# Kernel tuning notes

Measured on AMD Instinct MI355X. Metric: run time of the kernel, lower is better.

Reference implementation:

```python
import jax, jax.numpy as jnp
import numpy as np


def setup_inputs() -> dict:
    key = jax.random.key(0)
    k1, k2, k3, k4 = jax.random.split(key, 4)
    B, S, D = 32, 512, 768
    return {
        "image": jax.random.normal(k1, (B, S, D), dtype=jnp.float32),
        "text": jax.random.normal(k2, (B, S, D), dtype=jnp.float32),
        "target": jax.random.normal(k3, (B, S, D), dtype=jnp.float32),
        "padding_mask": jax.random.randint(k4, (B, S), 0, 2, dtype=jnp.int32),
    }


def reference(image, text, target, padding_mask):
    D = image.shape[-1]
    # Drop BOS / CLS position for the text<->target alignment.
    txt = text[:, 1:]                      # [B, S-1, D]
    tgt = target[:, 1:]                    # [B, S-1, D]
    pm = padding_mask[:, 1:]               # [B, S-1]

    # Cosine similarity: normalize then batched matmul.
    txt_n = txt / jnp.linalg.norm(txt, axis=-1, keepdims=True)
    tgt_n = tgt / jnp.linalg.norm(tgt, axis=-1, keepdims=True)
    sim = jnp.einsum('bid,bjd->bij', txt_n, tgt_n)   # [B, S-1, S-1]

    # For each text token, pick the best-matching target patch.
    idx = jnp.argmax(sim, axis=-1)                   # [B, S-1]
    aligned = jnp.take_along_axis(tgt, idx[..., None], axis=1)  # [B, S-1, D]

    # Masked MSE over non-padded tokens (mask==1 means padded in torch code).
    valid = (pm == 0).astype(jnp.float32)            # [B, S-1]
    diff2 = jnp.square(txt.astype(jnp.float32) - aligned.astype(jnp.float32))
    kd_text_loss = jnp.sum(diff2 * valid[..., None]) / (jnp.sum(valid) * D)

    # Plain MSE between image tokens and full target.
    kd_image_loss = jnp.mean(jnp.square(image.astype(jnp.float32) - target.astype(jnp.float32)))

    total_loss = (kd_text_loss + kd_image_loss) / 2
    return total_loss, kd_text_loss, kd_image_loss, idx
```

## Files before the change

kernel.cpp:

```cpp
#include <hip/hip_runtime.h>
#include <math.h>

#define B       32
#define S_FULL  512
#define S       511
#define D       768
#define NROWS   (B * S)

#define TM 128
#define TN 128
#define NCHUNK 4
#define NKT 24
#define RSTR 72
#define EPS_MARGIN 6e-5f

typedef __attribute__((ext_vector_type(8))) short bf16x8;
typedef __attribute__((ext_vector_type(4))) float f32x4;

__device__ inline unsigned short f2bf(float f) {
    union { float f; unsigned u; } c; c.f = f;
    unsigned u = c.u;
    return (unsigned short)((u + 0x7fffu + ((u >> 16) & 1u)) >> 16);
}
__device__ inline float bf2f(unsigned short h) {
    union { unsigned u; float f; } c; c.u = ((unsigned)h) << 16;
    return c.f;
}
__device__ inline void split4(float x0, float x1, float x2, float x3,
                              short4& hi, short4& lo) {
    unsigned short h0 = f2bf(x0), h1 = f2bf(x1), h2 = f2bf(x2), h3 = f2bf(x3);
    hi = make_short4((short)h0, (short)h1, (short)h2, (short)h3);
    lo = make_short4((short)f2bf(x0 - bf2f(h0)), (short)f2bf(x1 - bf2f(h1)),
                     (short)f2bf(x2 - bf2f(h2)), (short)f2bf(x3 - bf2f(h3)));
}

__global__ __launch_bounds__(256) void prep_kernel(
    const float* __restrict__ image, const float* __restrict__ text,
    const float* __restrict__ target,
    float* __restrict__ inv_t, float* __restrict__ inv_g, float* __restrict__ acc)
{
    int row  = blockIdx.x * 4 + (threadIdx.x >> 6);
    int lane = threadIdx.x & 63;
    int b = row >> 9, i = row & 511;
    const float4* pi4 = (const float4*)(image  + (size_t)row * D);
    const float4* pt4 = (const float4*)(text   + (size_t)row * D);
    const float4* pg4 = (const float4*)(target + (size_t)row * D);
    float st = 0.f, sg = 0.f, si = 0.f;
    #pragma unroll
    for (int q = 0; q < 3; ++q) {
        float4 a = pt4[lane + 64 * q];
        float4 g = pg4[lane + 64 * q];
        float4 m = pi4[lane + 64 * q];
        st += a.x*a.x + a.y*a.y + a.z*a.z + a.w*a.w;
        sg += g.x*g.x + g.y*g.y + g.z*g.z + g.w*g.w;
        float dx = m.x-g.x, dy = m.y-g.y, dz = m.z-g.z, dw = m.w-g.w;
        si += dx*dx + dy*dy + dz*dz + dw*dw;
    }
    #pragma unroll
    for (int m = 32; m > 0; m >>= 1) {
        st += __shfl_xor(st, m); sg += __shfl_xor(sg, m); si += __shfl_xor(si, m);
    }
    if (lane == 0) {
        atomicAdd(&acc[blockIdx.x & 63], si);
        if (i >= 1) {
            int r = b * S + i - 1;
            inv_t[r] = (st > 0.f) ? 1.f / sqrtf(st) : 0.f;
            inv_g[r] = (sg > 0.f) ? 1.f / sqrtf(sg) : 0.f;
        }
    }
}

__global__ __launch_bounds__(256, 2) void simargmax_kernel(
    const float* __restrict__ text, const float* __restrict__ target,
    const float* __restrict__ inv_t, const float* __restrict__ inv_g,
    float* __restrict__ pv, float* __restrict__ ps, int* __restrict__ pj)
{
    __shared__ __align__(16) short As[TM * RSTR];
    __shared__ __align__(16) short Bs[TM * RSTR];

    const int i0 = blockIdx.x * TM;
    const int jc = blockIdx.y;
    const int j0 = jc * TN;
    const int b  = blockIdx.z;
    const int t  = threadIdx.x;
    const int lane = t & 63;
    const int wy = t >> 6;
    const int quad = lane >> 4, cid = lane & 15;

    const float* Abase = text   + (size_t)b * S_FULL * D + D;
    const float* Bbase = target + (size_t)b * S_FULL * D + D;

    const int r0 = t >> 3;
    const int kq = (t & 7) * 4;

    float sa[4], sb[4];
    #pragma unroll
    for (int h = 0; h < 4; ++h) {
        int gi = i0 + r0 + h * 32;
        sa[h] = (gi < S) ? inv_t[b * S + gi] : 0.f;
        int gj = j0 + r0 + h * 32;
        sb[h] = (gj < S) ? inv_g[b * S + gj] : 0.f;
    }

    f32x4 acc[2][8];
    #pragma unroll
    for (int mt = 0; mt < 2; ++mt)
        #pragma unroll
        for (int nt = 0; nt < 8; ++nt)
            acc[mt][nt] = (f32x4){0.f, 0.f, 0.f, 0.f};

    for (int kt = 0; kt < NKT; ++kt) {
        const int k0 = kt * 32;
        float4 va[4], vb[4];
        #pragma unroll
        for (int h = 0; h < 4; ++h) {
            int gi = i0 + r0 + h * 32;
            va[h] = (gi < S) ? *(const float4*)(Abase + (size_t)gi * D + k0 + kq)
                             : make_float4(0.f, 0.f, 0.f, 0.f);
            int gj = j0 + r0 + h * 32;
            vb[h] = (gj < S) ? *(const float4*)(Bbase + (size_t)gj * D + k0 + kq)
                             : make_float4(0.f, 0.f, 0.f, 0.f);
        }
        __syncthreads();
        #pragma unroll
        for (int h = 0; h < 4; ++h) {
            int row = r0 + h * 32;
            short4 ahi, alo, bhi, blo;
            split4(va[h].x * sa[h], va[h].y * sa[h], va[h].z * sa[h], va[h].w * sa[h], ahi, alo);
            split4(vb[h].x * sb[h], vb[h].y * sb[h], vb[h].z * sb[h], vb[h].w * sb[h], bhi, blo);
            *(short4*)&As[row * RSTR + kq]      = ahi;
            *(short4*)&As[row * RSTR + 32 + kq] = alo;
            *(short4*)&Bs[row * RSTR + kq]      = bhi;
            *(short4*)&Bs[row * RSTR + 32 + kq] = blo;
        }
        __syncthreads();

        bf16x8 ah[2], al[2];
        #pragma unroll
        for (int mt = 0; mt < 2; ++mt) {
            int ad = (wy * 32 + mt * 16 + cid) * RSTR + quad * 8;
            ah[mt] = *(const bf16x8*)&As[ad];
            al[mt] = *(const bf16x8*)&As[ad + 32];
        }
        #pragma unroll
        for (int nt = 0; nt < 8; ++nt) {
            int bd = (nt * 16 + cid) * RSTR + quad * 8;
            bf16x8 bh = *(const bf16x8*)&Bs[bd];
            bf16x8 bl = *(const bf16x8*)&Bs[bd + 32];
            #pragma unroll
            for (int mt = 0; mt < 2; ++mt) {
                acc[mt][nt] = __builtin_amdgcn_mfma_f32_16x16x32_bf16(ah[mt], bh, acc[mt][nt], 0, 0, 0);
                acc[mt][nt] = __builtin_amdgcn_mfma_f32_16x16x32_bf16(ah[mt], bl, acc[mt][nt], 0, 0, 0);
                acc[mt][nt] = __builtin_amdgcn_mfma_f32_16x16x32_bf16(al[mt], bh, acc[mt][nt], 0, 0, 0);
            }
        }
    }

    #pragma unroll
    for (int mt = 0; mt < 2; ++mt) {
        #pragma unroll
        for (int r = 0; r < 4; ++r) {
            float v1 = -INFINITY, v2 = -INFINITY; int j1 = -1;
            #pragma unroll
            for (int nt = 0; nt < 8; ++nt) {
                int col = j0 + nt * 16 + cid;
                float v = acc[mt][nt][r];
                if (col < S) {
                    if (v > v1) { v2 = v1; v1 = v; j1 = col; }
                    else if (v > v2) v2 = v;
                }
            }
            #pragma unroll
            for (int m = 1; m < 16; m <<= 1) {
                float ov1 = __shfl_xor(v1, m);
                int   oj1 = __shfl_xor(j1, m);
                float ov2 = __shfl_xor(v2, m);
                if (ov1 > v1) { v2 = fmaxf(v1, ov2); v1 = ov1; j1 = oj1; }
                else          { v2 = fmaxf(v2, ov1); }
            }
            if (cid == 0) {
                int gi = i0 + wy * 32 + mt * 16 + quad * 4 + r;
                if (gi < S) {
                    size_t o = ((size_t)(b * S + gi) << 2) + jc;
                    pv[o] = v1; ps[o] = v2; pj[o] = j1;
                }
            }
        }
    }
}

__global__ __launch_bounds__(256) void text_kernel(
    const float* __restrict__ text, const float* __restrict__ target,
    const int* __restrict__ pm,
    const float* __restrict__ pv, const float* __restrict__ ps, const int* __restrict__ pj,
    float* __restrict__ idx_f, float* __restrict__ acc,
    int* __restrict__ list, int* __restrict__ cnt)
{
    int row = blockIdx.x * 4 + (threadIdx.x >> 6);
    if (row >= NROWS) return;
    int lane = threadIdx.x & 63;
    int b = row / S, i = row - b * S;

    float v1 = -INFINITY, v2 = -INFINITY; int j1 = 0;
    #pragma unroll
    for (int c = 0; c < NCHUNK; ++c) {
        size_t o = ((size_t)row << 2) + c;
        float a1 = pv[o], a2 = ps[o]; int aj = pj[o];
        if (a1 > v1) { v2 = fmaxf(v1, a2); v1 = a1; j1 = aj; }
        else         { v2 = fmaxf(v2, a1); }
    }
    if (v1 - v2 < EPS_MARGIN) {
        if (lane == 0) { int p = atomicAdd(cnt, 1); list[p] = row; }
        return;
    }
    if (lane == 0) idx_f[row] = (float)j1;

    if (pm[b * S_FULL + i + 1] != 0) return;
    const float4* pt = (const float4*)(text   + (size_t)(b * S_FULL + i  + 1) * D);
    const float4* pg = (const float4*)(target + (size_t)(b * S_FULL + j1 + 1) * D);
    float s = 0.f;
    #pragma unroll
    for (int q = 0; q < 3; ++q) {
        float4 a = pt[lane + 64 * q];
        float4 g = pg[lane + 64 * q];
        float dx = a.x-g.x, dy = a.y-g.y, dz = a.z-g.z, dw = a.w-g.w;
        s += dx*dx + dy*dy + dz*dz + dw*dw;
    }
    #pragma unroll
    for (int m = 32; m > 0; m >>= 1) s += __shfl_xor(s, m);
    if (lane == 0) {
        atomicAdd(&acc[64  + (blockIdx.x & 63)], s);
        atomicAdd(&acc[128 + (blockIdx.x & 63)], 1.0f);
    }
}

__global__ __launch_bounds__(256) void recheck_kernel(
    const float* __restrict__ text, const float* __restrict__ target,
    const int* __restrict__ pm, const float* __restrict__ inv_g,
    const int* __restrict__ list, const int* __restrict__ cnt,
    float* __restrict__ idx_f, float* __restrict__ acc)
{
    __shared__ float wv[4];
    __shared__ int   wj[4];
    __shared__ int   bjf;
    const int t = threadIdx.x, w = t >> 6, lane = t & 63;
    const int n = *cnt;
    for (int it = blockIdx.x; it < n; it += gridDim.x) {
        int row = list[it];
        int b = row / S, i = row - b * S;
        const float4* tp = (const float4*)(text + (size_t)(b * S_FULL + i + 1) * D);
        float4 tr0 = tp[lane], tr1 = tp[lane + 64], tr2 = tp[lane + 128];
        const float* Gb = target + (size_t)b * S_FULL * D + D;
        const float* ig = inv_g + b * S;

        float bv = -INFINITY; int bj = 0;
        for (int j = w; j < S; j += 8) {
            const float4* g0 = (const float4*)(Gb + (size_t)j * D);
            int j2 = j + 4; bool ok2 = (j2 < S);
            const float4* g1 = (const float4*)(Gb + (size_t)(ok2 ? j2 : j) * D);
            float4 a0 = g0[lane], a1 = g0[lane + 64], a2 = g0[lane + 128];
            float4 c0 = g1[lane], c1 = g1[lane + 64], c2 = g1[lane + 128];
            float s0 = tr0.x*a0.x + tr0.y*a0.y + tr0.z*a0.z + tr0.w*a0.w
                     + tr1.x*a1.x + tr1.y*a1.y + tr1.z*a1.z + tr1.w*a1.w
                     + tr2.x*a2.x + tr2.y*a2.y + tr2.z*a2.z + tr2.w*a2.w;
            float s1 = tr0.x*c0.x + tr0.y*c0.y + tr0.z*c0.z + tr0.w*c0.w
                     + tr1.x*c1.x + tr1.y*c1.y + tr1.z*c1.z + tr1.w*c1.w
                     + tr2.x*c2.x + tr2.y*c2.y + tr2.z*c2.z + tr2.w*c2.w;
            #pragma unroll
            for (int m = 32; m > 0; m >>= 1) {
                s0 += __shfl_xor(s0, m);
                s1 += __shfl_xor(s1, m);
            }
            s0 *= ig[j];
            if (s0 > bv) { bv = s0; bj = j; }
            if (ok2) {
                s1 *= ig[j2];
                if (s1 > bv) { bv = s1; bj = j2; }
            }
        }
        if (lane == 0) { wv[w] = bv; wj[w] = bj; }
        __syncthreads();
        if (t == 0) {
            float fv = wv[0]; int fj = wj[0];
            #pragma unroll
            for (int q = 1; q < 4; ++q)
                if (wv[q] > fv || (wv[q] == fv && wj[q] < fj)) { fv = wv[q]; fj = wj[q]; }
            bjf = fj;
            idx_f[row] = (float)fj;
        }
        __syncthreads();
        if (w == 0 && pm[b * S_FULL + i + 1] == 0) {
            const float4* gp = (const float4*)(Gb + (size_t)bjf * D);
            float4 a0 = gp[lane], a1 = gp[lane + 64], a2 = gp[lane + 128];
            float dx, s = 0.f;
            dx = tr0.x-a0.x; s += dx*dx;  dx = tr0.y-a0.y; s += dx*dx;
            dx = tr0.z-a0.z; s += dx*dx;  dx = tr0.w-a0.w; s += dx*dx;
            dx = tr1.x-a1.x; s += dx*dx;  dx = tr1.y-a1.y; s += dx*dx;
            dx = tr1.z-a1.z; s += dx*dx;  dx = tr1.w-a1.w; s += dx*dx;
            dx = tr2.x-a2.x; s += dx*dx;  dx = tr2.y-a2.y; s += dx*dx;
            dx = tr2.z-a2.z; s += dx*dx;  dx = tr2.w-a2.w; s += dx*dx;
            #pragma unroll
            for (int m = 32; m > 0; m >>= 1) s += __shfl_xor(s, m);
            if (lane == 0) {
                atomicAdd(&acc[64  + (blockIdx.x & 63)], s);
                atomicAdd(&acc[128 + (blockIdx.x & 63)], 1.0f);
            }
        }
        __syncthreads();
    }
}

__global__ void finalize_kernel(const float* __restrict__ acc, float* __restrict__ out)
{
    int lane = threadIdx.x;
    float si = acc[lane], st = acc[64 + lane], sc = acc[128 + lane];
    #pragma unroll
    for (int m = 32; m > 0; m >>= 1) {
        si += __shfl_xor(si, m);
        st += __shfl_xor(st, m);
        sc += __shfl_xor(sc, m);
    }
    if (lane == 0) {
        float img = si / (float)((size_t)B * S_FULL * D);
        float txt = st / (sc * (float)D);
        out[0] = 0.5f * (txt + img);
        out[1] = txt;
        out[2] = img;
    }
}

extern "C" void kernel_launch(void* const* d_in, const int* in_sizes, int n_in,
                              void* d_out, int out_size, void* d_ws, size_t ws_size,
                              hipStream_t stream) {
    const float* image  = (const float*)d_in[0];
    const float* text   = (const float*)d_in[1];
    const float* target = (const float*)d_in[2];
    const int*   pm     = (const int*)d_in[3];
    float* out = (float*)d_out;

    float* ws    = (float*)d_ws;
    float* inv_t = ws;
    float* inv_g = ws + NROWS;
    float* pv    = ws + 2 * NROWS;
    float* ps    = ws + 6 * NROWS;
    int*   pj    = (int*)(ws + 10 * NROWS);
    int*   list  = (int*)(ws + 14 * NROWS);
    int*   cnt   = (int*)(ws + 15 * NROWS);
    float* acc   = ws + 15 * NROWS + 64;

    hipMemsetAsync(ws + 15 * NROWS, 0, 256 * sizeof(float), stream);

    prep_kernel<<<B * S_FULL / 4, 256, 0, stream>>>(image, text, target, inv_t, inv_g, acc);
    simargmax_kernel<<<dim3(4, NCHUNK, B), 256, 0, stream>>>(
        text, target, inv_t, inv_g, pv, ps, pj);
    text_kernel<<<(NROWS + 3) / 4, 256, 0, stream>>>(
        text, target, pm, pv, ps, pj, out + 3, acc, list, cnt);
    recheck_kernel<<<512, 256, 0, stream>>>(
        text, target, pm, inv_g, list, cnt, out + 3, acc);
    finalize_kernel<<<1, 64, 0, stream>>>(acc, out);
}
```

Baseline: 355.6 us.

## Double-buffer LDS tiles in sim-argmax GEMM and fold finalize into recheck

The similarity GEMM now keeps two LDS buffers per operand. Global loads for the next k-tile are issued before the MFMAs on the current tile, and the bf16 hi/lo split is stored afterwards, so each iteration needs one barrier instead of two. The bf16 splitting now packs results straight into uint2 words. The separate finalize kernel is removed, and the last recheck block to finish (found through an atomic done counter) does the final reduction, which saves a launch. The cost is double the shared memory, which may lower occupancy, and more live registers.

```diff
diff --git a/kernel.cpp b/kernel.cpp
--- a/kernel.cpp
+++ b/kernel.cpp
@@ -17,21 +17,21 @@
 typedef __attribute__((ext_vector_type(8))) short bf16x8;
 typedef __attribute__((ext_vector_type(4))) float f32x4;
 
-__device__ inline unsigned short f2bf(float f) {
-    union { float f; unsigned u; } c; c.f = f;
-    unsigned u = c.u;
-    return (unsigned short)((u + 0x7fffu + ((u >> 16) & 1u)) >> 16);
-}
-__device__ inline float bf2f(unsigned short h) {
-    union { unsigned u; float f; } c; c.u = ((unsigned)h) << 16;
-    return c.f;
-}
-__device__ inline void split4(float x0, float x1, float x2, float x3,
-                              short4& hi, short4& lo) {
-    unsigned short h0 = f2bf(x0), h1 = f2bf(x1), h2 = f2bf(x2), h3 = f2bf(x3);
-    hi = make_short4((short)h0, (short)h1, (short)h2, (short)h3);
-    lo = make_short4((short)f2bf(x0 - bf2f(h0)), (short)f2bf(x1 - bf2f(h1)),
-                     (short)f2bf(x2 - bf2f(h2)), (short)f2bf(x3 - bf2f(h3)));
+__device__ inline unsigned rne16(float f) {
+    unsigned u = __builtin_bit_cast(unsigned, f);
+    return (u + 0x7fffu + ((u >> 16) & 1u)) >> 16;
+}
+__device__ inline void pk_split(float4 v, float s, uint2& hi, uint2& lo) {
+    float a0 = v.x * s, a1 = v.y * s, a2 = v.z * s, a3 = v.w * s;
+    unsigned r0 = rne16(a0), r1 = rne16(a1), r2 = rne16(a2), r3 = rne16(a3);
+    hi = make_uint2(r0 | (r1 << 16), r2 | (r3 << 16));
+    float f0 = __builtin_bit_cast(float, r0 << 16);
+    float f1 = __builtin_bit_cast(float, r1 << 16);
+    float f2 = __builtin_bit_cast(float, r2 << 16);
+    float f3 = __builtin_bit_cast(float, r3 << 16);
+    unsigned l0 = rne16(a0 - f0), l1 = rne16(a1 - f1);
+    unsigned l2 = rne16(a2 - f2), l3 = rne16(a3 - f3);
+    lo = make_uint2(l0 | (l1 << 16), l2 | (l3 << 16));
 }
 
 __global__ __launch_bounds__(256) void prep_kernel(
@@ -75,8 +75,8 @@
     const float* __restrict__ inv_t, const float* __restrict__ inv_g,
     float* __restrict__ pv, float* __restrict__ ps, int* __restrict__ pj)
 {
-    __shared__ __align__(16) short As[TM * RSTR];
-    __shared__ __align__(16) short Bs[TM * RSTR];
+    __shared__ __align__(16) short As[2][TM * RSTR];
+    __shared__ __align__(16) short Bs[2][TM * RSTR];
 
     const int i0 = blockIdx.x * TM;
     const int jc = blockIdx.y;
@@ -102,16 +102,9 @@
         sb[h] = (gj < S) ? inv_g[b * S + gj] : 0.f;
     }
 
-    f32x4 acc[2][8];
-    #pragma unroll
-    for (int mt = 0; mt < 2; ++mt)
-        #pragma unroll
-        for (int nt = 0; nt < 8; ++nt)
-            acc[mt][nt] = (f32x4){0.f, 0.f, 0.f, 0.f};
-
-    for (int kt = 0; kt < NKT; ++kt) {
+    float4 va[4], vb[4];
+    auto load_regs = [&](int kt) {
         const int k0 = kt * 32;
-        float4 va[4], vb[4];
         #pragma unroll
         for (int h = 0; h < 4; ++h) {
             int gi = i0 + r0 + h * 32;
@@ -121,32 +114,48 @@
             vb[h] = (gj < S) ? *(const float4*)(Bbase + (size_t)gj * D + k0 + kq)
                              : make_float4(0.f, 0.f, 0.f, 0.f);
         }
-        __syncthreads();
+    };
+    auto convert_store = [&](int buf) {
         #pragma unroll
         for (int h = 0; h < 4; ++h) {
             int row = r0 + h * 32;
-            short4 ahi, alo, bhi, blo;
-            split4(va[h].x * sa[h], va[h].y * sa[h], va[h].z * sa[h], va[h].w * sa[h], ahi, alo);
-            split4(vb[h].x * sb[h], vb[h].y * sb[h], vb[h].z * sb[h], vb[h].w * sb[h], bhi, blo);
-            *(short4*)&As[row * RSTR + kq]      = ahi;
-            *(short4*)&As[row * RSTR + 32 + kq] = alo;
-            *(short4*)&Bs[row * RSTR + kq]      = bhi;
-            *(short4*)&Bs[row * RSTR + 32 + kq] = blo;
-        }
-        __syncthreads();
+            uint2 hi, lo;
+            pk_split(va[h], sa[h], hi, lo);
+            *(uint2*)&As[buf][row * RSTR + kq]      = hi;
+            *(uint2*)&As[buf][row * RSTR + 32 + kq] = lo;
+            pk_split(vb[h], sb[h], hi, lo);
+            *(uint2*)&Bs[buf][row * RSTR + kq]      = hi;
+            *(uint2*)&Bs[buf][row * RSTR + 32 + kq] = lo;
+        }
+    };
+
+    f32x4 acc[2][8];
+    #pragma unroll
+    for (int mt = 0; mt < 2; ++mt)
+        #pragma unroll
+        for (int nt = 0; nt < 8; ++nt)
+            acc[mt][nt] = (f32x4){0.f, 0.f, 0.f, 0.f};
+
+    load_regs(0);
+    convert_store(0);
+    __syncthreads();
+
+    for (int kt = 0; kt < NKT; ++kt) {
+        const int cur = kt & 1;
+        if (kt + 1 < NKT) load_regs(kt + 1);
 
         bf16x8 ah[2], al[2];
         #pragma unroll
         for (int mt = 0; mt < 2; ++mt) {
             int ad = (wy * 32 + mt * 16 + cid) * RSTR + quad * 8;
-            ah[mt] = *(const bf16x8*)&As[ad];
-            al[mt] = *(const bf16x8*)&As[ad + 32];
+            ah[mt] = *(const bf16x8*)&As[cur][ad];
+            al[mt] = *(const bf16x8*)&As[cur][ad + 32];
         }
         #pragma unroll
         for (int nt = 0; nt < 8; ++nt) {
             int bd = (nt * 16 + cid) * RSTR + quad * 8;
-            bf16x8 bh = *(const bf16x8*)&Bs[bd];
-            bf16x8 bl = *(const bf16x8*)&Bs[bd + 32];
+            bf16x8 bh = *(const bf16x8*)&Bs[cur][bd];
+            bf16x8 bl = *(const bf16x8*)&Bs[cur][bd + 32];
             #pragma unroll
             for (int mt = 0; mt < 2; ++mt) {
                 acc[mt][nt] = __builtin_amdgcn_mfma_f32_16x16x32_bf16(ah[mt], bh, acc[mt][nt], 0, 0, 0);
@@ -154,6 +163,8 @@
                 acc[mt][nt] = __builtin_amdgcn_mfma_f32_16x16x32_bf16(al[mt], bh, acc[mt][nt], 0, 0, 0);
             }
         }
+        if (kt + 1 < NKT) convert_store(cur ^ 1);
+        __syncthreads();
     }
 
     #pragma unroll
@@ -238,11 +249,13 @@
     const float* __restrict__ text, const float* __restrict__ target,
     const int* __restrict__ pm, const float* __restrict__ inv_g,
     const int* __restrict__ list, const int* __restrict__ cnt,
-    float* __restrict__ idx_f, float* __restrict__ acc)
+    float* __restrict__ idx_f, float* __restrict__ acc,
+    int* __restrict__ done, float* __restrict__ out)
 {
     __shared__ float wv[4];
     __shared__ int   wj[4];
     __shared__ int   bjf;
+    __shared__ int   lastFlag;
     const int t = threadIdx.x, w = t >> 6, lane = t & 63;
     const int n = *cnt;
     for (int it = blockIdx.x; it < n; it += gridDim.x) {
@@ -308,24 +321,30 @@
         }
         __syncthreads();
     }
-}
-
-__global__ void finalize_kernel(const float* __restrict__ acc, float* __restrict__ out)
-{
-    int lane = threadIdx.x;
-    float si = acc[lane], st = acc[64 + lane], sc = acc[128 + lane];
-    #pragma unroll
-    for (int m = 32; m > 0; m >>= 1) {
-        si += __shfl_xor(si, m);
-        st += __shfl_xor(st, m);
-        sc += __shfl_xor(sc, m);
-    }
-    if (lane == 0) {
-        float img = si / (float)((size_t)B * S_FULL * D);
-        float txt = st / (sc * (float)D);
-        out[0] = 0.5f * (txt + img);
-        out[1] = txt;
-        out[2] = img;
+
+    if (t == 0) {
+        __threadfence();
+        int p = atomicAdd(done, 1);
+        lastFlag = (p == (int)gridDim.x - 1);
+    }
+    __syncthreads();
+    if (lastFlag && t < 64) {
+        float si = atomicAdd(&acc[t], 0.0f);
+        float st = atomicAdd(&acc[64 + t], 0.0f);
+        float sc = atomicAdd(&acc[128 + t], 0.0f);
+        #pragma unroll
+        for (int m = 32; m > 0; m >>= 1) {
+            si += __shfl_xor(si, m);
+            st += __shfl_xor(st, m);
+            sc += __shfl_xor(sc, m);
+        }
+        if (t == 0) {
+            float img = si / (float)((size_t)B * S_FULL * D);
+            float txt = st / (sc * (float)D);
+            out[0] = 0.5f * (txt + img);
+            out[1] = txt;
+            out[2] = img;
+        }
     }
 }
 
@@ -345,10 +364,12 @@
     float* ps    = ws + 6 * NROWS;
     int*   pj    = (int*)(ws + 10 * NROWS);
     int*   list  = (int*)(ws + 14 * NROWS);
-    int*   cnt   = (int*)(ws + 15 * NROWS);
-    float* acc   = ws + 15 * NROWS + 64;
-
-    hipMemsetAsync(ws + 15 * NROWS, 0, 256 * sizeof(float), stream);
+    float* zs    = ws + 15 * NROWS;
+    int*   cnt   = (int*)zs;
+    int*   done  = (int*)zs + 1;
+    float* acc   = zs + 64;
+
+    (void)hipMemsetAsync(zs, 0, 256 * sizeof(float), stream);
 
     prep_kernel<<<B * S_FULL / 4, 256, 0, stream>>>(image, text, target, inv_t, inv_g, acc);
     simargmax_kernel<<<dim3(4, NCHUNK, B), 256, 0, stream>>>(
@@ -356,6 +377,5 @@
     text_kernel<<<(NROWS + 3) / 4, 256, 0, stream>>>(
         text, target, pm, pv, ps, pj, out + 3, acc, list, cnt);
     recheck_kernel<<<512, 256, 0, stream>>>(
-        text, target, pm, inv_g, list, cnt, out + 3, acc);
-    finalize_kernel<<<1, 64, 0, stream>>>(acc, out);
-}
+        text, target, pm, inv_g, list, cnt, out + 3, acc, done, out);
+}
```

New measurement: 361.1 us. Within noise of the previous version (+1.5%).
